# Kernel optimization log

Hardware: AMD Instinct MI355X
Metric: run time of the kernel (lower is better)

## Reference

```python
import jax, jax.numpy as jnp
import numpy as np

N_HEADS = 16
HEAD_DIM = 128
ROPE_DIM = 64
ROPE_BASE = 10000.0


def _rope(x, base):
    # x: (B, H, S, dim) -- standard rotate-half RoPE, positions = arange(S)
    B, H, S, dim = x.shape
    inv_freq = 1.0 / (base ** (jnp.arange(0, dim, 2, dtype=jnp.float32) / dim))
    pos = jnp.arange(S, dtype=jnp.float32)
    freqs = pos[:, None] * inv_freq[None, :]                  # (S, dim/2)
    emb = jnp.concatenate([freqs, freqs], axis=-1)            # (S, dim)
    cos = jnp.cos(emb).astype(x.dtype)[None, None]
    sin = jnp.sin(emb).astype(x.dtype)[None, None]
    x1, x2 = x[..., : dim // 2], x[..., dim // 2 :]
    rot = jnp.concatenate([-x2, x1], axis=-1)
    return x * cos + rot * sin


def setup_inputs() -> dict:
    key = jax.random.key(0)
    ks = jax.random.split(key, 7)
    B, S, D = 2, 2048, 2048
    s = 0.02
    return {
        "x": jax.random.normal(ks[0], (B, S, D), jnp.float32),
        "Wq": jax.random.normal(ks[1], (D, N_HEADS * HEAD_DIM), jnp.float32) * s,
        "Wq_rope": jax.random.normal(ks[2], (D, N_HEADS * ROPE_DIM), jnp.float32) * s,
        "Wkv_down": jax.random.normal(ks[3], (D, 512), jnp.float32) * s,
        "Wkv_up": jax.random.normal(ks[4], (512, 2 * N_HEADS * HEAD_DIM), jnp.float32) * s,
        "Wk_rope": jax.random.normal(ks[5], (D, ROPE_DIM), jnp.float32) * s,
        "Wo": jax.random.normal(ks[6], (D, D), jnp.float32) * s,
    }


def reference(x, Wq, Wq_rope, Wkv_down, Wkv_up, Wk_rope, Wo):
    B, S, D = x.shape
    H, hd, rd = N_HEADS, HEAD_DIM, ROPE_DIM

    # content and decoupled-RoPE queries
    q_c = (x @ Wq).reshape(B, S, H, hd).transpose(0, 2, 1, 3)        # (B,H,S,hd)
    q_r = (x @ Wq_rope).reshape(B, S, H, rd).transpose(0, 2, 1, 3)   # (B,H,S,rd)
    q_r = _rope(q_r, ROPE_BASE)

    # low-rank KV latent + shared rope key
    c_kv = x @ Wkv_down                                              # (B,S,r)
    k_r = _rope((x @ Wk_rope)[:, None, :, :], ROPE_BASE)             # (B,1,S,rd)

    kv = c_kv @ Wkv_up                                               # (B,S,2*H*hd)
    k_c, v = jnp.split(kv, 2, axis=-1)
    k_c = k_c.reshape(B, S, H, hd).transpose(0, 2, 1, 3)             # (B,H,S,hd)
    v = v.reshape(B, S, H, hd).transpose(0, 2, 1, 3)                 # (B,H,S,hd)

    q_full = jnp.concatenate([q_c, q_r], axis=-1)                    # (B,H,S,hd+rd)
    k_full = jnp.concatenate([k_c, jnp.broadcast_to(k_r, (B, H, S, rd))], axis=-1)

    scale = 1.0 / np.sqrt(hd + rd).astype(np.float32)
    scores = jnp.einsum("bhqd,bhkd->bhqk", q_full, k_full) * scale   # (B,H,S,S)
    mask = jnp.tril(jnp.ones((S, S), dtype=bool))
    scores = jnp.where(mask[None, None], scores, jnp.finfo(scores.dtype).min)
    attn = jax.nn.softmax(scores, axis=-1)

    out = jnp.einsum("bhqk,bhkd->bhqd", attn, v)                     # (B,H,S,hd)
    out = out.transpose(0, 2, 1, 3).reshape(B, S, D)
    return out @ Wo
```

## Files before the change

kernel.cpp:

```cpp
#include <hip/hip_runtime.h>
#include <hip/hip_bf16.h>
#include <cstdint>
#include <cstddef>

typedef unsigned short u16;
typedef __attribute__((ext_vector_type(8))) short short8;
typedef __attribute__((ext_vector_type(4))) float f32x4;

__device__ __forceinline__ u16 f2bf(float f) {
    union { float f; uint32_t u; } v; v.f = f;
    uint32_t u = v.u;
    return (u16)((u + 0x7fffu + ((u >> 16) & 1u)) >> 16);
}
__device__ __forceinline__ float bf2f(u16 u) {
    union { uint32_t u; float f; } v; v.u = ((uint32_t)u) << 16;
    return v.f;
}

__device__ __forceinline__ void async_cp16(const u16* g, u16* l) {
    __builtin_amdgcn_global_load_lds(
        (const __attribute__((address_space(1))) unsigned int*)g,
        (__attribute__((address_space(3))) unsigned int*)l, 16, 0, 0);
}

__global__ __launch_bounds__(256) void cast_f32_bf16(const float* __restrict__ in,
                                                     u16* __restrict__ out, int n) {
    int i = (blockIdx.x * 256 + threadIdx.x) * 4;
    if (i >= n) return;
    float4 v = *(const float4*)(in + i);
    ushort4 r;
    r.x = f2bf(v.x); r.y = f2bf(v.y); r.z = f2bf(v.z); r.w = f2bf(v.w);
    *(ushort4*)(out + i) = r;
}

__global__ __launch_bounds__(256) void transpose_cast(const float* __restrict__ W,
                                                      u16* __restrict__ Wt, int K, int N,
                                                      float smul) {
    __shared__ u16 tile[64][72];
    int kt = blockIdx.x * 64, nt = blockIdx.y * 64;
    int t = threadIdx.x;
#pragma unroll
    for (int i = 0; i < 16; i++) {
        int idx = t + i * 256; int kl = idx >> 6, nl = idx & 63;
        tile[kl][nl] = f2bf(W[(size_t)(kt + kl) * N + nt + nl] * smul);
    }
    __syncthreads();
#pragma unroll
    for (int i = 0; i < 16; i++) {
        int idx = t + i * 256; int nl = idx >> 6, kl = idx & 63;
        Wt[(size_t)(nt + nl) * K + kt + kl] = tile[kl][nl];
    }
}

template <int OUTF32, int KDIM, int NDIM>
__global__ __launch_bounds__(256) void gemm_bt(const u16* __restrict__ A, int lda,
                                               const u16* __restrict__ Bt,
                                               void* __restrict__ Cout, int ldc) {
    __shared__ __align__(16) u16 Al[128 * 32];
    __shared__ __align__(16) u16 Bl[128 * 32];
    int m0 = blockIdx.x * 128, n0 = blockIdx.y * 128;
    int t = threadIdx.x;
    int w = t >> 6, l = t & 63;
    int lm = l & 15, lq = l >> 4;
    int wm = (w >> 1) * 64, wn = (w & 1) * 64;
    f32x4 acc[4][4] = {};

    for (int k0 = 0; k0 < KDIM; k0 += 32) {
#pragma unroll
        for (int c = 0; c < 2; c++) {
            int chunk = w * 128 + c * 64 + l;
            int row = chunk >> 2, col8 = (chunk & 3) * 8;
            async_cp16(A + (size_t)(m0 + row) * lda + k0 + col8,
                       Al + (w * 128 + c * 64) * 8);
            int brow = n0 + row;
            if (NDIM % 128 != 0) { if (brow >= NDIM) brow = NDIM - 1; }
            async_cp16(Bt + (size_t)brow * KDIM + k0 + col8,
                       Bl + (w * 128 + c * 64) * 8);
        }
        __syncthreads();
        short8 af[4], bfr[4];
#pragma unroll
        for (int mt = 0; mt < 4; mt++)
            af[mt] = *(const short8*)(Al + (wm + mt * 16 + lm) * 32 + lq * 8);
#pragma unroll
        for (int nt = 0; nt < 4; nt++)
            bfr[nt] = *(const short8*)(Bl + (wn + nt * 16 + lm) * 32 + lq * 8);
#pragma unroll
        for (int mt = 0; mt < 4; mt++)
#pragma unroll
            for (int nt = 0; nt < 4; nt++)
                acc[mt][nt] = __builtin_amdgcn_mfma_f32_16x16x32_bf16(af[mt], bfr[nt], acc[mt][nt], 0, 0, 0);
        __syncthreads();
    }
#pragma unroll
    for (int mt = 0; mt < 4; mt++) {
#pragma unroll
        for (int nt = 0; nt < 4; nt++) {
            int col = n0 + wn + nt * 16 + lm;
            if (col < NDIM) {
#pragma unroll
                for (int r = 0; r < 4; r++) {
                    int row = m0 + wm + mt * 16 + lq * 4 + r;
                    if (OUTF32) ((float*)Cout)[(size_t)row * ldc + col] = acc[mt][nt][r];
                    else        ((u16*)Cout)[(size_t)row * ldc + col] = f2bf(acc[mt][nt][r]);
                }
            }
        }
    }
}

__global__ __launch_bounds__(256) void rope_kernel(u16* __restrict__ x, int rows,
                                                   int nheads, int Smask, int stride) {
    int i = blockIdx.x * 256 + threadIdx.x;
    int total = rows * nheads * 32;
    if (i >= total) return;
    int j = i & 31;
    int h = (i >> 5) % nheads;
    int row = i / (32 * nheads);
    int pos = row & Smask;
    float f = exp2f((float)j * -0.4152410118609828f);
    float ang = (float)pos * f;
    float c = cosf(ang), s = sinf(ang);
    u16* p = x + (size_t)row * stride + h * 64 + j;
    float x1 = bf2f(p[0]), x2 = bf2f(p[32]);
    p[0]  = f2bf(x1 * c - x2 * s);
    p[32] = f2bf(x2 * c + x1 * s);
}

__global__ __launch_bounds__(256) void transpose_v(const u16* __restrict__ kv,
                                                   u16* __restrict__ vt, int S) {
    __shared__ u16 tile[64][72];
    int bh = blockIdx.z; int b = bh >> 4, h = bh & 15;
    int s0 = blockIdx.x * 64, d0 = blockIdx.y * 64;
    int t = threadIdx.x;
#pragma unroll
    for (int i = 0; i < 16; i++) {
        int idx = t + i * 256; int sl = idx >> 6, dl = idx & 63;
        tile[sl][dl] = kv[(size_t)(b * S + s0 + sl) * 4096 + 2048 + h * 128 + d0 + dl];
    }
    __syncthreads();
#pragma unroll
    for (int i = 0; i < 16; i++) {
        int idx = t + i * 256; int dl = idx >> 6, sl = idx & 63;
        vt[((size_t)(bh * 128 + d0 + dl)) * S + s0 + sl] = tile[sl][dl];
    }
}

__global__ __launch_bounds__(256) void mla_attn(const u16* __restrict__ qc, int qcs,
                                                const u16* __restrict__ qr, int qrs,
                                                const u16* __restrict__ kvbuf,
                                                const u16* __restrict__ kr, int krs,
                                                const u16* __restrict__ vt,
                                                u16* __restrict__ out, int S) {
    __shared__ __align__(16) u16 Kl[64 * 200];
    __shared__ __align__(16) u16 Vl[128 * 72];
    __shared__ __align__(16) u16 Plds[4][16 * 72];
    int bh = blockIdx.x; int b = bh >> 4, h = bh & 15;
    int qt = 31 - (int)blockIdx.y;
    int t = threadIdx.x, w = t >> 6, l = t & 63;
    int lm = l & 15, lq = l >> 4;

    short8 kreg[6], vreg[4];
    auto load_tile = [&](int kbase) {
#pragma unroll
        for (int c = 0; c < 6; c++) {
            int idx = t + c * 256;
            int row = idx / 24, col = (idx % 24) * 8;
            const u16* src = (col < 128)
                ? kvbuf + (size_t)(b * S + kbase + row) * 4096 + h * 128 + col
                : kr + (size_t)(b * S + kbase + row) * krs + (col - 128);
            kreg[c] = *(const short8*)src;
        }
#pragma unroll
        for (int c = 0; c < 4; c++) {
            int idx = t + c * 256;
            int row = idx >> 3, col = (idx & 7) * 8;
            vreg[c] = *(const short8*)(vt + ((size_t)bh * 128 + row) * S + kbase + col);
        }
    };

    int qrow = qt * 64 + w * 16;
    int ntiles = qt + 1;

    short8 bq[6];
    {
        const u16* qc_row = qc + (size_t)(b * S + qrow + lm) * qcs + h * 128;
#pragma unroll
        for (int ks = 0; ks < 4; ks++) bq[ks] = *(const short8*)(qc_row + ks * 32 + lq * 8);
        const u16* qr_row = qr + (size_t)(b * S + qrow + lm) * qrs + h * 64;
#pragma unroll
        for (int ks = 0; ks < 2; ks++) bq[4 + ks] = *(const short8*)(qr_row + ks * 32 + lq * 8);
    }

    f32x4 o[8] = {};
    float m_s = -INFINITY, l_s = 0.f;

    load_tile(0);
    for (int kt = 0; kt < ntiles; kt++) {
        int kbase = kt * 64;
        __syncthreads();
#pragma unroll
        for (int c = 0; c < 6; c++) {
            int idx = t + c * 256;
            int row = idx / 24, col = (idx % 24) * 8;
            *(short8*)(Kl + row * 200 + col) = kreg[c];
        }
#pragma unroll
        for (int c = 0; c < 4; c++) {
            int idx = t + c * 256;
            int row = idx >> 3, col = (idx & 7) * 8;
            *(short8*)(Vl + row * 72 + col) = vreg[c];
        }
        __syncthreads();
        if (kt + 1 < ntiles) load_tile(kbase + 64);

        if (kbase > qrow + 15) continue;

        f32x4 acc[4] = {};
        __builtin_amdgcn_s_setprio(1);
#pragma unroll
        for (int ks = 0; ks < 6; ks++) {
#pragma unroll
            for (int mt = 0; mt < 4; mt++) {
                short8 ak = *(const short8*)(Kl + (mt * 16 + lm) * 200 + ks * 32 + lq * 8);
                acc[mt] = __builtin_amdgcn_mfma_f32_16x16x32_bf16(ak, bq[ks], acc[mt], 0, 0, 0);
            }
        }
        __builtin_amdgcn_s_setprio(0);
        if (kbase + 63 > qrow) {
            int qi = qrow + lm;
#pragma unroll
            for (int mt = 0; mt < 4; mt++)
#pragma unroll
                for (int r = 0; r < 4; r++) {
                    int ki = kbase + mt * 16 + lq * 4 + r;
                    if (ki > qi) acc[mt][r] = -INFINITY;
                }
        }
        float mx = -INFINITY;
#pragma unroll
        for (int mt = 0; mt < 4; mt++)
#pragma unroll
            for (int r = 0; r < 4; r++) mx = fmaxf(mx, acc[mt][r]);
        mx = fmaxf(mx, __shfl_xor(mx, 16));
        mx = fmaxf(mx, __shfl_xor(mx, 32));
        if (!__all(mx - m_s <= 8.0f)) {
            float mnew = fmaxf(m_s, mx);
            float alpha = exp2f(m_s - mnew);
            m_s = mnew;
            l_s *= alpha;
#pragma unroll
            for (int mt = 0; mt < 8; mt++)
#pragma unroll
                for (int r = 0; r < 4; r++) o[mt][r] *= alpha;
        }

        u16* pl = Plds[w];
        float rs = 0.f;
#pragma unroll
        for (int mt = 0; mt < 4; mt++) {
            float p0 = exp2f(acc[mt][0] - m_s);
            float p1 = exp2f(acc[mt][1] - m_s);
            float p2 = exp2f(acc[mt][2] - m_s);
            float p3 = exp2f(acc[mt][3] - m_s);
            rs += (p0 + p1) + (p2 + p3);
            ushort4 pk; pk.x = f2bf(p0); pk.y = f2bf(p1); pk.z = f2bf(p2); pk.w = f2bf(p3);
            *(ushort4*)(pl + lm * 72 + mt * 16 + lq * 4) = pk;
        }
        rs += __shfl_xor(rs, 16);
        rs += __shfl_xor(rs, 32);
        l_s += rs;

        __builtin_amdgcn_s_setprio(1);
#pragma unroll
        for (int ks2 = 0; ks2 < 2; ks2++) {
            short8 bp = *(const short8*)(pl + lm * 72 + ks2 * 32 + lq * 8);
#pragma unroll
            for (int mt = 0; mt < 8; mt++) {
                short8 av = *(const short8*)(Vl + (mt * 16 + lm) * 72 + ks2 * 32 + lq * 8);
                o[mt] = __builtin_amdgcn_mfma_f32_16x16x32_bf16(av, bp, o[mt], 0, 0, 0);
            }
        }
        __builtin_amdgcn_s_setprio(0);
    }
    float inv = 1.0f / l_s;
    u16* orow = out + (size_t)(b * S + qrow + lm) * 2048 + h * 128;
#pragma unroll
    for (int mt = 0; mt < 8; mt++) {
        ushort4 pk;
        pk.x = f2bf(o[mt][0] * inv);
        pk.y = f2bf(o[mt][1] * inv);
        pk.z = f2bf(o[mt][2] * inv);
        pk.w = f2bf(o[mt][3] * inv);
        *(ushort4*)(orow + mt * 16 + lq * 4) = pk;
    }
}

extern "C" void kernel_launch(void* const* d_in, const int* in_sizes, int n_in,
                              void* d_out, int out_size, void* d_ws, size_t ws_size,
                              hipStream_t stream) {
    const int B = 2, S = 2048, D = 2048, H = 16;
    const int M = B * S;
    const int NP = 3648;
    const int NPpad = 3712;
    const float scale = 0.07216878364870323f * 1.4426950408889634f;
    const float* x    = (const float*)d_in[0];
    const float* Wq   = (const float*)d_in[1];
    const float* Wqr  = (const float*)d_in[2];
    const float* Wkvd = (const float*)d_in[3];
    const float* Wkvu = (const float*)d_in[4];
    const float* Wkr  = (const float*)d_in[5];
    const float* Wo   = (const float*)d_in[6];

    u16* p = (u16*)d_ws;
    u16* xb     = p; p += (size_t)M * D;
    u16* WprojT = p; p += (size_t)NPpad * 2048;
    u16* WkvuT  = p; p += (size_t)4096 * 512;
    u16* WoT    = p; p += (size_t)2048 * 2048;
    u16* proj   = p; p += (size_t)M * NPpad;
    u16* kv     = p; p += (size_t)M * 4096;
    u16* v_t    = p; p += (size_t)B * H * 128 * S;
    u16* attn   = p; p += (size_t)M * 2048;

    u16* q_c = proj;
    u16* q_r = proj + 2048;
    u16* ckv = proj + 3072;
    u16* k_r = proj + 3584;

    cast_f32_bf16<<<(M * D) / 4 / 256, 256, 0, stream>>>(x, xb, M * D);
    transpose_cast<<<dim3(32, 32), 256, 0, stream>>>(Wq,   WprojT,               2048, 2048, scale);
    transpose_cast<<<dim3(32, 16), 256, 0, stream>>>(Wqr,  WprojT + 2048 * 2048, 2048, 1024, scale);
    transpose_cast<<<dim3(32, 8),  256, 0, stream>>>(Wkvd, WprojT + 3072 * 2048, 2048, 512, 1.0f);
    transpose_cast<<<dim3(32, 1),  256, 0, stream>>>(Wkr,  WprojT + 3584 * 2048, 2048, 64, 1.0f);
    transpose_cast<<<dim3(8, 64),  256, 0, stream>>>(Wkvu, WkvuT, 512, 4096, 1.0f);
    transpose_cast<<<dim3(32, 32), 256, 0, stream>>>(Wo,   WoT,   2048, 2048, 1.0f);

    gemm_bt<0, 2048, NP><<<dim3(32, 29), 256, 0, stream>>>(xb, 2048, WprojT, proj, NPpad);

    rope_kernel<<<(M * 16 * 32) / 256, 256, 0, stream>>>(q_r, M, 16, S - 1, NPpad);
    rope_kernel<<<(M * 32) / 256, 256, 0, stream>>>(k_r, M, 1, S - 1, NPpad);

    gemm_bt<0, 512, 4096><<<dim3(32, 32), 256, 0, stream>>>(ckv, NPpad, WkvuT, kv, 4096);
    transpose_v<<<dim3(32, 2, 32), 256, 0, stream>>>(kv, v_t, S);

    mla_attn<<<dim3(32, 32), 256, 0, stream>>>(q_c, NPpad, q_r, NPpad, kv, k_r, NPpad,
                                               v_t, attn, S);

    gemm_bt<1, 2048, 2048><<<dim3(32, 16), 256, 0, stream>>>(attn, 2048, WoT, d_out, 2048);
}
```

Measured before the change: 423.1 us.

## Use 32x32 MFMA with 128-row query tiles and register-resident P in attention

Rewrites the attention kernel to use 32x32x16 bf16 MFMA instructions. Each block now covers 128 query rows (32 per wave) instead of 64, which halves the number of blocks and doubles K/V reuse per loaded tile. The softmax probabilities now stay in registers and are rearranged with cross-lane shuffles instead of going through a shared-memory P buffer. The query tile order is changed to pair long and short causal tiles, and launch bounds request two blocks per CU. Register pressure rises and there are fewer blocks to fill the GPU, and the running max now starts at 0 instead of -inf.

Result: no change. 418.6 us (-1.1%).

```diff
diff --git a/kernel.cpp b/kernel.cpp
--- a/kernel.cpp
+++ b/kernel.cpp
@@ -6,6 +6,7 @@
 typedef unsigned short u16;
 typedef __attribute__((ext_vector_type(8))) short short8;
 typedef __attribute__((ext_vector_type(4))) float f32x4;
+typedef __attribute__((ext_vector_type(16))) float f32x16;
 
 __device__ __forceinline__ u16 f2bf(float f) {
     union { float f; uint32_t u; } v; v.f = f;
@@ -15,6 +16,9 @@
 __device__ __forceinline__ float bf2f(u16 u) {
     union { uint32_t u; float f; } v; v.u = ((uint32_t)u) << 16;
     return v.f;
+}
+__device__ __forceinline__ uint32_t pk2(float lo, float hi) {
+    return (uint32_t)f2bf(lo) | ((uint32_t)f2bf(hi) << 16);
 }
 
 __device__ __forceinline__ void async_cp16(const u16* g, u16* l) {
@@ -146,19 +150,20 @@
     }
 }
 
-__global__ __launch_bounds__(256) void mla_attn(const u16* __restrict__ qc, int qcs,
-                                                const u16* __restrict__ qr, int qrs,
-                                                const u16* __restrict__ kvbuf,
-                                                const u16* __restrict__ kr, int krs,
-                                                const u16* __restrict__ vt,
-                                                u16* __restrict__ out, int S) {
+__global__ __launch_bounds__(256, 2) void mla_attn(const u16* __restrict__ qc, int qcs,
+                                                   const u16* __restrict__ qr, int qrs,
+                                                   const u16* __restrict__ kvbuf,
+                                                   const u16* __restrict__ kr, int krs,
+                                                   const u16* __restrict__ vt,
+                                                   u16* __restrict__ out, int S) {
     __shared__ __align__(16) u16 Kl[64 * 200];
     __shared__ __align__(16) u16 Vl[128 * 72];
-    __shared__ __align__(16) u16 Plds[4][16 * 72];
+    const float NEG = -1e30f;
     int bh = blockIdx.x; int b = bh >> 4, h = bh & 15;
-    int qt = 31 - (int)blockIdx.y;
+    int y = blockIdx.y;
+    int qt = (y < 8) ? (15 - y) : (y - 8);
     int t = threadIdx.x, w = t >> 6, l = t & 63;
-    int lm = l & 15, lq = l >> 4;
+    int ln = l & 31, hi = l >> 5;
 
     short8 kreg[6], vreg[4];
     auto load_tile = [&](int kbase) {
@@ -179,21 +184,21 @@
         }
     };
 
-    int qrow = qt * 64 + w * 16;
-    int ntiles = qt + 1;
-
-    short8 bq[6];
+    int qrow = qt * 128 + w * 32;
+    int ntiles = 2 * qt + 2;
+
+    short8 bq[12];
     {
-        const u16* qc_row = qc + (size_t)(b * S + qrow + lm) * qcs + h * 128;
-#pragma unroll
-        for (int ks = 0; ks < 4; ks++) bq[ks] = *(const short8*)(qc_row + ks * 32 + lq * 8);
-        const u16* qr_row = qr + (size_t)(b * S + qrow + lm) * qrs + h * 64;
-#pragma unroll
-        for (int ks = 0; ks < 2; ks++) bq[4 + ks] = *(const short8*)(qr_row + ks * 32 + lq * 8);
-    }
-
-    f32x4 o[8] = {};
-    float m_s = -INFINITY, l_s = 0.f;
+        const u16* qc_row = qc + (size_t)(b * S + qrow + ln) * qcs + h * 128;
+#pragma unroll
+        for (int ks = 0; ks < 8; ks++) bq[ks] = *(const short8*)(qc_row + ks * 16 + hi * 8);
+        const u16* qr_row = qr + (size_t)(b * S + qrow + ln) * qrs + h * 64;
+#pragma unroll
+        for (int ks = 0; ks < 4; ks++) bq[8 + ks] = *(const short8*)(qr_row + ks * 16 + hi * 8);
+    }
+
+    f32x16 o[4] = {};
+    float m_s = 0.0f, l_s = 0.f;
 
     load_tile(0);
     for (int kt = 0; kt < ntiles; kt++) {
@@ -214,35 +219,35 @@
         __syncthreads();
         if (kt + 1 < ntiles) load_tile(kbase + 64);
 
-        if (kbase > qrow + 15) continue;
-
-        f32x4 acc[4] = {};
+        if (kbase > qrow + 31) continue;
+
+        f32x16 sacc[2] = {};
         __builtin_amdgcn_s_setprio(1);
 #pragma unroll
-        for (int ks = 0; ks < 6; ks++) {
-#pragma unroll
-            for (int mt = 0; mt < 4; mt++) {
-                short8 ak = *(const short8*)(Kl + (mt * 16 + lm) * 200 + ks * 32 + lq * 8);
-                acc[mt] = __builtin_amdgcn_mfma_f32_16x16x32_bf16(ak, bq[ks], acc[mt], 0, 0, 0);
-            }
+        for (int ks = 0; ks < 12; ks++) {
+            short8 ak0 = *(const short8*)(Kl + ln * 200 + ks * 16 + hi * 8);
+            short8 ak1 = *(const short8*)(Kl + (32 + ln) * 200 + ks * 16 + hi * 8);
+            sacc[0] = __builtin_amdgcn_mfma_f32_32x32x16_bf16(ak0, bq[ks], sacc[0], 0, 0, 0);
+            sacc[1] = __builtin_amdgcn_mfma_f32_32x32x16_bf16(ak1, bq[ks], sacc[1], 0, 0, 0);
         }
         __builtin_amdgcn_s_setprio(0);
+
         if (kbase + 63 > qrow) {
-            int qi = qrow + lm;
-#pragma unroll
-            for (int mt = 0; mt < 4; mt++)
-#pragma unroll
-                for (int r = 0; r < 4; r++) {
-                    int ki = kbase + mt * 16 + lq * 4 + r;
-                    if (ki > qi) acc[mt][r] = -INFINITY;
+            int qi = qrow + ln;
+#pragma unroll
+            for (int kt2 = 0; kt2 < 2; kt2++)
+#pragma unroll
+                for (int r = 0; r < 16; r++) {
+                    int key = kbase + kt2 * 32 + (r & 3) + 8 * (r >> 2) + 4 * hi;
+                    if (key > qi) sacc[kt2][r] = NEG;
                 }
         }
-        float mx = -INFINITY;
-#pragma unroll
-        for (int mt = 0; mt < 4; mt++)
-#pragma unroll
-            for (int r = 0; r < 4; r++) mx = fmaxf(mx, acc[mt][r]);
-        mx = fmaxf(mx, __shfl_xor(mx, 16));
+
+        float mx = NEG;
+#pragma unroll
+        for (int kt2 = 0; kt2 < 2; kt2++)
+#pragma unroll
+            for (int r = 0; r < 16; r++) mx = fmaxf(mx, sacc[kt2][r]);
         mx = fmaxf(mx, __shfl_xor(mx, 32));
         if (!__all(mx - m_s <= 8.0f)) {
             float mnew = fmaxf(m_s, mx);
@@ -250,50 +255,68 @@
             m_s = mnew;
             l_s *= alpha;
 #pragma unroll
-            for (int mt = 0; mt < 8; mt++)
-#pragma unroll
-                for (int r = 0; r < 4; r++) o[mt][r] *= alpha;
-        }
-
-        u16* pl = Plds[w];
+            for (int dt = 0; dt < 4; dt++) o[dt] *= alpha;
+        }
+
         float rs = 0.f;
-#pragma unroll
-        for (int mt = 0; mt < 4; mt++) {
-            float p0 = exp2f(acc[mt][0] - m_s);
-            float p1 = exp2f(acc[mt][1] - m_s);
-            float p2 = exp2f(acc[mt][2] - m_s);
-            float p3 = exp2f(acc[mt][3] - m_s);
-            rs += (p0 + p1) + (p2 + p3);
-            ushort4 pk; pk.x = f2bf(p0); pk.y = f2bf(p1); pk.z = f2bf(p2); pk.w = f2bf(p3);
-            *(ushort4*)(pl + lm * 72 + mt * 16 + lq * 4) = pk;
-        }
-        rs += __shfl_xor(rs, 16);
+        short8 bp[2][2];
+#pragma unroll
+        for (int kt2 = 0; kt2 < 2; kt2++) {
+            float p[16];
+#pragma unroll
+            for (int r = 0; r < 16; r++) p[r] = exp2f(sacc[kt2][r] - m_s);
+#pragma unroll
+            for (int r = 0; r < 16; r++) rs += p[r];
+            uint32_t c0 = pk2(p[0], p[1]),  c1 = pk2(p[2], p[3]);
+            uint32_t c2 = pk2(p[4], p[5]),  c3 = pk2(p[6], p[7]);
+            uint32_t e0 = __shfl_xor(c0, 32), e1 = __shfl_xor(c1, 32);
+            uint32_t e2 = __shfl_xor(c2, 32), e3 = __shfl_xor(c3, 32);
+            union { uint32_t u[4]; short8 s; } f0;
+            f0.u[0] = hi ? e2 : c0;
+            f0.u[1] = hi ? e3 : c1;
+            f0.u[2] = hi ? c2 : e0;
+            f0.u[3] = hi ? c3 : e1;
+            bp[kt2][0] = f0.s;
+            uint32_t c4 = pk2(p[8], p[9]),   c5 = pk2(p[10], p[11]);
+            uint32_t c6 = pk2(p[12], p[13]), c7 = pk2(p[14], p[15]);
+            uint32_t e4 = __shfl_xor(c4, 32), e5 = __shfl_xor(c5, 32);
+            uint32_t e6 = __shfl_xor(c6, 32), e7 = __shfl_xor(c7, 32);
+            union { uint32_t u[4]; short8 s; } f1;
+            f1.u[0] = hi ? e6 : c4;
+            f1.u[1] = hi ? e7 : c5;
+            f1.u[2] = hi ? c6 : e4;
+            f1.u[3] = hi ? c7 : e5;
+            bp[kt2][1] = f1.s;
+        }
         rs += __shfl_xor(rs, 32);
         l_s += rs;
 
         __builtin_amdgcn_s_setprio(1);
 #pragma unroll
-        for (int ks2 = 0; ks2 < 2; ks2++) {
-            short8 bp = *(const short8*)(pl + lm * 72 + ks2 * 32 + lq * 8);
-#pragma unroll
-            for (int mt = 0; mt < 8; mt++) {
-                short8 av = *(const short8*)(Vl + (mt * 16 + lm) * 72 + ks2 * 32 + lq * 8);
-                o[mt] = __builtin_amdgcn_mfma_f32_16x16x32_bf16(av, bp, o[mt], 0, 0, 0);
-            }
-        }
+        for (int kt2 = 0; kt2 < 2; kt2++)
+#pragma unroll
+            for (int s = 0; s < 2; s++)
+#pragma unroll
+                for (int dt = 0; dt < 4; dt++) {
+                    short8 av = *(const short8*)(Vl + (dt * 32 + ln) * 72 + kt2 * 32 + s * 16 + hi * 8);
+                    o[dt] = __builtin_amdgcn_mfma_f32_32x32x16_bf16(av, bp[kt2][s], o[dt], 0, 0, 0);
+                }
         __builtin_amdgcn_s_setprio(0);
     }
+
     float inv = 1.0f / l_s;
-    u16* orow = out + (size_t)(b * S + qrow + lm) * 2048 + h * 128;
-#pragma unroll
-    for (int mt = 0; mt < 8; mt++) {
-        ushort4 pk;
-        pk.x = f2bf(o[mt][0] * inv);
-        pk.y = f2bf(o[mt][1] * inv);
-        pk.z = f2bf(o[mt][2] * inv);
-        pk.w = f2bf(o[mt][3] * inv);
-        *(ushort4*)(orow + mt * 16 + lq * 4) = pk;
-    }
+    u16* orow = out + (size_t)(b * S + qrow + ln) * 2048 + h * 128;
+#pragma unroll
+    for (int dt = 0; dt < 4; dt++)
+#pragma unroll
+        for (int g = 0; g < 4; g++) {
+            ushort4 pk4;
+            pk4.x = f2bf(o[dt][g * 4 + 0] * inv);
+            pk4.y = f2bf(o[dt][g * 4 + 1] * inv);
+            pk4.z = f2bf(o[dt][g * 4 + 2] * inv);
+            pk4.w = f2bf(o[dt][g * 4 + 3] * inv);
+            *(ushort4*)(orow + dt * 32 + g * 8 + hi * 4) = pk4;
+        }
 }
 
 extern "C" void kernel_launch(void* const* d_in, const int* in_sizes, int n_in,
@@ -343,7 +366,7 @@
     gemm_bt<0, 512, 4096><<<dim3(32, 32), 256, 0, stream>>>(ckv, NPpad, WkvuT, kv, 4096);
     transpose_v<<<dim3(32, 2, 32), 256, 0, stream>>>(kv, v_t, S);
 
-    mla_attn<<<dim3(32, 32), 256, 0, stream>>>(q_c, NPpad, q_r, NPpad, kv, k_r, NPpad,
+    mla_attn<<<dim3(32, 16), 256, 0, stream>>>(q_c, NPpad, q_r, NPpad, kv, k_r, NPpad,
                                                v_t, attn, S);
 
     gemm_bt<1, 2048, 2048><<<dim3(32, 16), 256, 0, stream>>>(attn, 2048, WoT, d_out, 2048);
```
